# Kernel tuning notes

Hardware: AMD Instinct MI355X
Metric: run time of the kernel (lower is better)

The kernel has to match this reference:

```python
import jax, jax.numpy as jnp
import numpy as np
import math

D_MODEL = 1024
N_HEADS = 16
HEAD_DIM = D_MODEL // N_HEADS
BATCH = 2
SEQ = 2048


def setup_inputs() -> dict:
    key = jax.random.key(0)
    ks = jax.random.split(key, 6)
    x = jax.random.normal(ks[0], (BATCH, SEQ, D_MODEL), dtype=jnp.float32)
    # causal additive mask, finite large negative
    causal = jnp.tril(jnp.ones((SEQ, SEQ), dtype=bool))
    attn_mask = jnp.where(causal, 0.0, -1e9).astype(jnp.float32)[None, None, :, :]
    s = 1.0 / math.sqrt(D_MODEL)
    W_qkv = jax.random.uniform(ks[1], (3 * D_MODEL, D_MODEL), jnp.float32, -s, s)
    b_qkv = jax.random.uniform(ks[2], (3 * D_MODEL,), jnp.float32, -s, s)
    W_out = jax.random.uniform(ks[3], (D_MODEL, D_MODEL), jnp.float32, -s, s)
    b_out = jax.random.uniform(ks[4], (D_MODEL,), jnp.float32, -s, s)
    return {"x": x, "attn_mask": attn_mask, "W_qkv": W_qkv, "b_qkv": b_qkv,
            "W_out": W_out, "b_out": b_out}


def reference(x, attn_mask, W_qkv, b_qkv, W_out, b_out):
    batch, seq, _ = x.shape
    # torch Linear: x @ W^T + b
    qkv = x @ W_qkv.T + b_qkv                              # [B,S,3D]
    qkv = qkv.reshape(batch, seq, 3, N_HEADS, HEAD_DIM)
    qkv = jnp.transpose(qkv, (2, 0, 3, 1, 4))              # [3,B,H,S,hd]
    q, k, v = qkv[0], qkv[1], qkv[2]
    scores = jnp.einsum('bhsd,bhtd->bhst', q, k) / math.sqrt(HEAD_DIM)
    scores = scores + attn_mask
    attn = jax.nn.softmax(scores, axis=-1)                 # dropout p=0 (eval)
    context = jnp.einsum('bhst,bhtd->bhsd', attn, v)       # [B,H,S,hd]
    context = jnp.transpose(context, (0, 2, 1, 3)).reshape(batch, seq, D_MODEL)
    return context @ W_out.T + b_out
```

## Files before the change

### kernel.cpp

```cpp
#include <hip/hip_runtime.h>
#include <hip/hip_bf16.h>

#define BATCH 2
#define SEQ 2048
#define DMODEL 1024
#define NHEADS 16
#define HDIM 64
#define MROWS (BATCH*SEQ)

typedef short bf16x8_t __attribute__((ext_vector_type(8)));
typedef float f32x4_t __attribute__((ext_vector_type(4)));

union Frag { uint4 u; bf16x8_t b; };

__device__ __forceinline__ unsigned short f2bf(float f) {
  union { __hip_bfloat16 h; unsigned short s; } u;
  u.h = __float2bfloat16(f);
  return u.s;
}

__device__ __forceinline__ void gload16(const unsigned short* g, unsigned short* l) {
  __builtin_amdgcn_global_load_lds(
      (const __attribute__((address_space(1))) unsigned int*)(const void*)g,
      (__attribute__((address_space(3))) unsigned int*)(void*)l,
      16, 0, 0);
}

__global__ void cvt_kernel(const float* __restrict__ in,
                           unsigned short* __restrict__ out, int n4) {
  for (int i = blockIdx.x * blockDim.x + threadIdx.x; i < n4;
       i += gridDim.x * blockDim.x) {
    float4 v = reinterpret_cast<const float4*>(in)[i];
    ushort4 o;
    o.x = f2bf(v.x); o.y = f2bf(v.y); o.z = f2bf(v.z); o.w = f2bf(v.w);
    reinterpret_cast<ushort4*>(out)[i] = o;
  }
}

#define QSCALE 0.18033688011112042f


__launch_bounds__(256)
__global__ void qkv_gemm_kernel(const unsigned short* __restrict__ A,
                                const unsigned short* __restrict__ Bw,
                                const float* __restrict__ bias,
                                unsigned short* __restrict__ qb,
                                unsigned short* __restrict__ kb,
                                unsigned short* __restrict__ vb) {
  __shared__ __align__(16) unsigned short As[128 * 32];
  __shared__ __align__(16) unsigned short Bs[128 * 32];
  const int tid = threadIdx.x;
  const int w = tid >> 6, lane = tid & 63;
  const int rr = lane & 15, cg = lane >> 4;
  const int wr = w >> 1, wc = w & 1;
  const int bm = blockIdx.x * 128, bn = blockIdx.y * 128;

  const int cid0 = (w * 2) * 64 + lane, cid1 = (w * 2 + 1) * 64 + lane;
  const int rowA0 = cid0 >> 2, kc0 = cid0 & 3;
  const int rowA1 = cid1 >> 2, kc1 = cid1 & 3;
  const unsigned short* gA0 = A + (size_t)(bm + rowA0) * DMODEL + kc0 * 8;
  const unsigned short* gA1 = A + (size_t)(bm + rowA1) * DMODEL + kc1 * 8;
  const unsigned short* gB0 = Bw + (size_t)(bn + rowA0) * DMODEL + kc0 * 8;
  const unsigned short* gB1 = Bw + (size_t)(bn + rowA1) * DMODEL + kc1 * 8;
  unsigned short* lA0 = As + (w * 2) * 512;
  unsigned short* lA1 = As + (w * 2 + 1) * 512;
  unsigned short* lB0 = Bs + (w * 2) * 512;
  unsigned short* lB1 = Bs + (w * 2 + 1) * 512;

  f32x4_t acc[4][4];
#pragma unroll
  for (int i = 0; i < 4; ++i)
#pragma unroll
    for (int j = 0; j < 4; ++j) acc[i][j] = (f32x4_t){0.f, 0.f, 0.f, 0.f};

  for (int k0 = 0; k0 < DMODEL; k0 += 32) {
    __syncthreads();
    gload16(gA0 + k0, lA0);
    gload16(gA1 + k0, lA1);
    gload16(gB0 + k0, lB0);
    gload16(gB1 + k0, lB1);
    __syncthreads();
    const uint4* A4 = reinterpret_cast<const uint4*>(As);
    const uint4* B4 = reinterpret_cast<const uint4*>(Bs);
    Frag af[4], bf[4];
#pragma unroll
    for (int mt = 0; mt < 4; ++mt) af[mt].u = A4[(wr * 64 + 16 * mt + rr) * 4 + cg];
#pragma unroll
    for (int nt = 0; nt < 4; ++nt) bf[nt].u = B4[(wc * 64 + 16 * nt + rr) * 4 + cg];
#pragma unroll
    for (int mt = 0; mt < 4; ++mt)
#pragma unroll
      for (int nt = 0; nt < 4; ++nt)
        acc[mt][nt] = __builtin_amdgcn_mfma_f32_16x16x32_bf16(af[mt].b, bf[nt].b, acc[mt][nt], 0, 0, 0);
  }

#pragma unroll
  for (int nt = 0; nt < 4; ++nt) {
    const int m = bn + wc * 64 + 16 * nt + rr;
    const float bv = bias[m];
    const int which = m >> 10;
    const int h = (m & 1023) >> 6;
    const int d = m & 63;
#pragma unroll
    for (int mt = 0; mt < 4; ++mt) {
#pragma unroll
      for (int r = 0; r < 4; ++r) {
        const int n = bm + wr * 64 + 16 * mt + cg * 4 + r;
        const int b = n >> 11, sq = n & (SEQ - 1);
        const int bh = b * NHEADS + h;
        float val = acc[mt][nt][r] + bv;
        if (which == 0) {
          qb[((size_t)bh * SEQ + sq) * HDIM + d] = f2bf(val * QSCALE);
        } else if (which == 1) {
          kb[((size_t)bh * SEQ + sq) * HDIM + d] = f2bf(val);
        } else {
          vb[((size_t)bh * HDIM + d) * SEQ + sq] = f2bf(val);
        }
      }
    }
  }
}

__launch_bounds__(256)
__global__ void out_gemm_kernel(const unsigned short* __restrict__ A,
                                const unsigned short* __restrict__ Bw,
                                const float* __restrict__ bias,
                                float* __restrict__ out) {
  __shared__ __align__(16) unsigned short As[128 * 32];
  __shared__ __align__(16) unsigned short Bs[128 * 32];
  const int tid = threadIdx.x;
  const int w = tid >> 6, lane = tid & 63;
  const int rr = lane & 15, cg = lane >> 4;
  const int wr = w >> 1, wc = w & 1;
  const int bm = blockIdx.x * 128, bn = blockIdx.y * 128;

  const int cid0 = (w * 2) * 64 + lane, cid1 = (w * 2 + 1) * 64 + lane;
  const int rowA0 = cid0 >> 2, kc0 = cid0 & 3;
  const int rowA1 = cid1 >> 2, kc1 = cid1 & 3;
  const unsigned short* gA0 = A + (size_t)(bm + rowA0) * DMODEL + kc0 * 8;
  const unsigned short* gA1 = A + (size_t)(bm + rowA1) * DMODEL + kc1 * 8;
  const unsigned short* gB0 = Bw + (size_t)(bn + rowA0) * DMODEL + kc0 * 8;
  const unsigned short* gB1 = Bw + (size_t)(bn + rowA1) * DMODEL + kc1 * 8;
  unsigned short* lA0 = As + (w * 2) * 512;
  unsigned short* lA1 = As + (w * 2 + 1) * 512;
  unsigned short* lB0 = Bs + (w * 2) * 512;
  unsigned short* lB1 = Bs + (w * 2 + 1) * 512;

  f32x4_t acc[4][4];
#pragma unroll
  for (int i = 0; i < 4; ++i)
#pragma unroll
    for (int j = 0; j < 4; ++j) acc[i][j] = (f32x4_t){0.f, 0.f, 0.f, 0.f};

  for (int k0 = 0; k0 < DMODEL; k0 += 32) {
    __syncthreads();
    gload16(gA0 + k0, lA0);
    gload16(gA1 + k0, lA1);
    gload16(gB0 + k0, lB0);
    gload16(gB1 + k0, lB1);
    __syncthreads();
    const uint4* A4 = reinterpret_cast<const uint4*>(As);
    const uint4* B4 = reinterpret_cast<const uint4*>(Bs);
    Frag af[4], bf[4];
#pragma unroll
    for (int mt = 0; mt < 4; ++mt) af[mt].u = A4[(wr * 64 + 16 * mt + rr) * 4 + cg];
#pragma unroll
    for (int nt = 0; nt < 4; ++nt) bf[nt].u = B4[(wc * 64 + 16 * nt + rr) * 4 + cg];
#pragma unroll
    for (int mt = 0; mt < 4; ++mt)
#pragma unroll
      for (int nt = 0; nt < 4; ++nt)
        acc[mt][nt] = __builtin_amdgcn_mfma_f32_16x16x32_bf16(af[mt].b, bf[nt].b, acc[mt][nt], 0, 0, 0);
  }

#pragma unroll
  for (int nt = 0; nt < 4; ++nt) {
    const int m = bn + wc * 64 + 16 * nt + rr;
    const float bv = bias[m];
#pragma unroll
    for (int mt = 0; mt < 4; ++mt) {
#pragma unroll
      for (int r = 0; r < 4; ++r) {
        const int n = bm + wr * 64 + 16 * mt + cg * 4 + r;
        out[(size_t)n * DMODEL + m] = acc[mt][nt][r] + bv;
      }
    }
  }
}

__launch_bounds__(256, 4)
__global__ void attn_kernel(const unsigned short* __restrict__ qb,
                            const unsigned short* __restrict__ kb,
                            const unsigned short* __restrict__ vb,
                            unsigned short* __restrict__ ctx) {
  __shared__ __align__(16) uint4 Ks[2][512];
  __shared__ __align__(16) uint4 Vs[2][512];

  const int tid = threadIdx.x;
  const int w = tid >> 6, lane = tid & 63;
  const int rr = lane & 15, cg = lane >> 4;
  const int rxw = rr & 7;
  const int bh = blockIdx.x;
  const int c = 31 - blockIdx.y;

  const unsigned short* Kbh = kb + (size_t)bh * SEQ * HDIM;
  const unsigned short* Vbh = vb + (size_t)bh * HDIM * SEQ;

  const int j0 = w * 2, j1 = w * 2 + 1;
  const int cid0 = j0 * 64 + lane, cid1 = j1 * 64 + lane;
  const int row0 = cid0 >> 3, ch0 = cid0 & 7;
  const int row1 = cid1 >> 3, ch1 = cid1 & 7;
  const int kOff0 = row0 * HDIM + ((ch0 ^ (row0 & 7)) << 3);
  const int kOff1 = row1 * HDIM + ((ch1 ^ (row1 & 7)) << 3);
  const int vOff0 = row0 * SEQ + ((ch0 ^ (row0 & 7)) << 3);
  const int vOff1 = row1 * SEQ + ((ch1 ^ (row1 & 7)) << 3);

#define STAGE(bi, tb_) do {                                             \
    const unsigned short* Kt_ = Kbh + (size_t)(tb_) * HDIM;             \
    const unsigned short* Vt_ = Vbh + (tb_);                            \
    unsigned short* kl_ = (unsigned short*)&Ks[bi][0];                  \
    unsigned short* vl_ = (unsigned short*)&Vs[bi][0];                  \
    gload16(Kt_ + kOff0, kl_ + j0 * 512);                               \
    gload16(Kt_ + kOff1, kl_ + j1 * 512);                               \
    gload16(Vt_ + vOff0, vl_ + j0 * 512);                               \
    gload16(Vt_ + vOff1, vl_ + j1 * 512);                               \
  } while (0)

  const int b = bh >> 4, h = bh & 15;
  const int s_base = c * 64 + w * 16;
  const int nt = c + 1;

  STAGE(0, 0);

  Frag q0, q1;
  {
    const unsigned short* qrow = qb + ((size_t)bh * SEQ + (s_base + rr)) * HDIM;
    q0.u = *reinterpret_cast<const uint4*>(qrow + cg * 8);
    q1.u = *reinterpret_cast<const uint4*>(qrow + 32 + cg * 8);
  }

  f32x4_t acc[4];
#pragma unroll
  for (int i = 0; i < 4; ++i) acc[i] = (f32x4_t){0.f, 0.f, 0.f, 0.f};
  float mreg = -1e30f;
  float lp = 0.f;

  for (int t = 0; t < nt; ++t) {
    __syncthreads();
    if (t + 1 < nt) STAGE((t + 1) & 1, (t + 1) * 64);
    const uint4* Kt = &Ks[t & 1][0];
    const uint4* Vt = &Vs[t & 1][0];

    f32x4_t s[4];
    __builtin_amdgcn_s_setprio(1);
#pragma unroll
    for (int st = 0; st < 4; ++st) {
      s[st] = (f32x4_t){0.f, 0.f, 0.f, 0.f};
      Frag kf;
      kf.u = Kt[(st * 16 + rr) * 8 + (cg ^ rxw)];
      s[st] = __builtin_amdgcn_mfma_f32_16x16x32_bf16(kf.b, q0.b, s[st], 0, 0, 0);
      kf.u = Kt[(st * 16 + rr) * 8 + ((4 + cg) ^ rxw)];
      s[st] = __builtin_amdgcn_mfma_f32_16x16x32_bf16(kf.b, q1.b, s[st], 0, 0, 0);
    }
    __builtin_amdgcn_s_setprio(0);

    if (t == nt - 1) {
#pragma unroll
      for (int st = 0; st < 4; ++st)
#pragma unroll
        for (int r = 0; r < 4; ++r)
          if (st * 16 + cg * 4 + r > w * 16 + rr) s[st][r] = -1e30f;
    }

    float mx = s[0][0];
#pragma unroll
    for (int st = 0; st < 4; ++st)
#pragma unroll
      for (int r = 0; r < 4; ++r) mx = fmaxf(mx, s[st][r]);
    if (__any(mx > mreg + 11.0f)) {
      float m = fmaxf(mx, __shfl_xor(mx, 16));
      m = fmaxf(m, __shfl_xor(m, 32));
      m = fmaxf(m, mreg);
      const float alpha = exp2f(mreg - m);
      mreg = m;
      lp *= alpha;
      float av[4];
#pragma unroll
      for (int r = 0; r < 4; ++r) av[r] = __shfl(alpha, cg * 4 + r);
#pragma unroll
      for (int dt = 0; dt < 4; ++dt)
#pragma unroll
        for (int r = 0; r < 4; ++r) acc[dt][r] *= av[r];
    }

    float pv[4][4];
#pragma unroll
    for (int st = 0; st < 4; ++st)
#pragma unroll
      for (int r = 0; r < 4; ++r) {
        pv[st][r] = exp2f(s[st][r] - mreg);
        lp += pv[st][r];
      }

    unsigned int uu[4][2];
#pragma unroll
    for (int st = 0; st < 4; ++st)
#pragma unroll
      for (int i = 0; i < 2; ++i)
        asm("v_cvt_pk_bf16_f32 %0, %1, %2"
            : "=v"(uu[st][i]) : "v"(pv[st][2 * i]), "v"(pv[st][2 * i + 1]));

    Frag pA0, pA1;
#pragma unroll
    for (int s2 = 0; s2 < 2; ++s2) {
#pragma unroll
      for (int i = 0; i < 2; ++i) {
        unsigned int x = uu[2 * s2][i], y = uu[2 * s2 + 1][i];
        asm("v_permlane32_swap_b32 %0, %1" : "+v"(x), "+v"(y));
        asm("v_permlane16_swap_b32 %0, %1" : "+v"(x), "+v"(y));
        if (s2 == 0) { pA0.u[i] = x; pA0.u[2 + i] = y; }
        else         { pA1.u[i] = x; pA1.u[2 + i] = y; }
      }
    }

    __builtin_amdgcn_s_setprio(1);
#pragma unroll
    for (int dt = 0; dt < 4; ++dt) {
      Frag vf;
      vf.u = Vt[(dt * 16 + rr) * 8 + (cg ^ rxw)];
      acc[dt] = __builtin_amdgcn_mfma_f32_16x16x32_bf16(pA0.b, vf.b, acc[dt], 0, 0, 0);
      vf.u = Vt[(dt * 16 + rr) * 8 + ((4 + cg) ^ rxw)];
      acc[dt] = __builtin_amdgcn_mfma_f32_16x16x32_bf16(pA1.b, vf.b, acc[dt], 0, 0, 0);
    }
    __builtin_amdgcn_s_setprio(0);
  }

  float ls = lp + __shfl_xor(lp, 16);
  ls += __shfl_xor(ls, 32);
  const float inv = 1.0f / ls;
  float iv[4];
#pragma unroll
  for (int r = 0; r < 4; ++r) iv[r] = __shfl(inv, cg * 4 + r);
#pragma unroll
  for (int r = 0; r < 4; ++r) {
    const int sq = s_base + cg * 4 + r;
    unsigned short* crow = ctx + (size_t)(b * SEQ + sq) * DMODEL + h * HDIM;
#pragma unroll
    for (int dt = 0; dt < 4; ++dt)
      crow[dt * 16 + rr] = f2bf(acc[dt][r] * iv[r]);
  }
#undef STAGE
}

extern "C" void kernel_launch(void* const* d_in, const int* in_sizes, int n_in,
                              void* d_out, int out_size, void* d_ws, size_t ws_size,
                              hipStream_t stream) {
  const float* x    = (const float*)d_in[0];
  const float* Wqkv = (const float*)d_in[2];
  const float* bqkv = (const float*)d_in[3];
  const float* Wout = (const float*)d_in[4];
  const float* bout = (const float*)d_in[5];
  float* out = (float*)d_out;

  unsigned short* ws    = (unsigned short*)d_ws;
  unsigned short* xb    = ws;
  unsigned short* wqkvb = xb + (size_t)MROWS * DMODEL;
  unsigned short* woutb = wqkvb + (size_t)3 * DMODEL * DMODEL;
  unsigned short* qbuf  = woutb + (size_t)DMODEL * DMODEL;
  unsigned short* kbuf  = qbuf + (size_t)BATCH * NHEADS * SEQ * HDIM;
  unsigned short* vbuf  = kbuf + (size_t)BATCH * NHEADS * SEQ * HDIM;
  unsigned short* ctx   = vbuf + (size_t)BATCH * NHEADS * SEQ * HDIM;

  cvt_kernel<<<1024, 256, 0, stream>>>(x, xb, MROWS * DMODEL / 4);
  cvt_kernel<<<1024, 256, 0, stream>>>(Wqkv, wqkvb, 3 * DMODEL * DMODEL / 4);
  cvt_kernel<<<256, 256, 0, stream>>>(Wout, woutb, DMODEL * DMODEL / 4);

  qkv_gemm_kernel<<<dim3(MROWS / 128, 3 * DMODEL / 128), 256, 0, stream>>>(
      xb, wqkvb, bqkv, qbuf, kbuf, vbuf);

  attn_kernel<<<dim3(BATCH * NHEADS, SEQ / 64), 256, 0, stream>>>(
      qbuf, kbuf, vbuf, ctx);

  out_gemm_kernel<<<dim3(MROWS / 128, DMODEL / 128), 256, 0, stream>>>(
      ctx, woutb, bout, out);
}
```

Measured before the change: 114.8 us.

## Halve attention block size, load V from global, fuse conversion kernels

The attention kernel now uses 128-thread blocks covering 32 query rows, so there are twice as many blocks and causal work is balanced more finely. V tiles are no longer staged through LDS: each wave reads its V fragments straight from global memory into registers, and K staging is rebalanced across two waves. The row max uses v_max3 and the probability buffer reuses the score registers. The three fp32-to-bf16 conversion launches become one kernel with branching on index. The risks are uncoalesced, per-wave redundant global V loads and extra K reloads per query row.

```diff
diff --git a/kernel.cpp b/kernel.cpp
--- a/kernel.cpp
+++ b/kernel.cpp
@@ -19,6 +19,12 @@
   return u.s;
 }
 
+__device__ __forceinline__ float max3f(float a, float b, float c) {
+  float d;
+  asm("v_max3_f32 %0, %1, %2, %3" : "=v"(d) : "v"(a), "v"(b), "v"(c));
+  return d;
+}
+
 __device__ __forceinline__ void gload16(const unsigned short* g, unsigned short* l) {
   __builtin_amdgcn_global_load_lds(
       (const __attribute__((address_space(1))) unsigned int*)(const void*)g,
@@ -26,14 +32,22 @@
       16, 0, 0);
 }
 
-__global__ void cvt_kernel(const float* __restrict__ in,
-                           unsigned short* __restrict__ out, int n4) {
-  for (int i = blockIdx.x * blockDim.x + threadIdx.x; i < n4;
+__global__ void cvt3_kernel(const float* __restrict__ a, const float* __restrict__ b,
+                            const float* __restrict__ c,
+                            unsigned short* __restrict__ oa, unsigned short* __restrict__ ob,
+                            unsigned short* __restrict__ oc,
+                            int na, int nb, int nc) {
+  const int n = na + nb + nc;
+  for (int i = blockIdx.x * blockDim.x + threadIdx.x; i < n;
        i += gridDim.x * blockDim.x) {
-    float4 v = reinterpret_cast<const float4*>(in)[i];
+    const float* src; unsigned short* dst; int j;
+    if (i < na)           { src = a; dst = oa; j = i; }
+    else if (i < na + nb) { src = b; dst = ob; j = i - na; }
+    else                  { src = c; dst = oc; j = i - na - nb; }
+    float4 v = reinterpret_cast<const float4*>(src)[j];
     ushort4 o;
     o.x = f2bf(v.x); o.y = f2bf(v.y); o.z = f2bf(v.z); o.w = f2bf(v.w);
-    reinterpret_cast<ushort4*>(out)[i] = o;
+    reinterpret_cast<ushort4*>(dst)[j] = o;
   }
 }
 
@@ -188,47 +202,44 @@
   }
 }
 
-__launch_bounds__(256, 4)
+__launch_bounds__(128, 4)
 __global__ void attn_kernel(const unsigned short* __restrict__ qb,
                             const unsigned short* __restrict__ kb,
                             const unsigned short* __restrict__ vb,
                             unsigned short* __restrict__ ctx) {
   __shared__ __align__(16) uint4 Ks[2][512];
-  __shared__ __align__(16) uint4 Vs[2][512];
 
   const int tid = threadIdx.x;
   const int w = tid >> 6, lane = tid & 63;
   const int rr = lane & 15, cg = lane >> 4;
   const int rxw = rr & 7;
   const int bh = blockIdx.x;
-  const int c = 31 - blockIdx.y;
+  const int h = 63 - blockIdx.y;
+  const int b = bh >> 4, hd = bh & 15;
 
   const unsigned short* Kbh = kb + (size_t)bh * SEQ * HDIM;
   const unsigned short* Vbh = vb + (size_t)bh * HDIM * SEQ;
 
-  const int j0 = w * 2, j1 = w * 2 + 1;
-  const int cid0 = j0 * 64 + lane, cid1 = j1 * 64 + lane;
-  const int row0 = cid0 >> 3, ch0 = cid0 & 7;
-  const int row1 = cid1 >> 3, ch1 = cid1 & 7;
-  const int kOff0 = row0 * HDIM + ((ch0 ^ (row0 & 7)) << 3);
-  const int kOff1 = row1 * HDIM + ((ch1 ^ (row1 & 7)) << 3);
-  const int vOff0 = row0 * SEQ + ((ch0 ^ (row0 & 7)) << 3);
-  const int vOff1 = row1 * SEQ + ((ch1 ^ (row1 & 7)) << 3);
+  int kOff[4];
+#pragma unroll
+  for (int j = 0; j < 4; ++j) {
+    const int cid = (2 * j + w) * 64 + lane;
+    const int row = cid >> 3, ch = cid & 7;
+    kOff[j] = row * HDIM + ((ch ^ (row & 7)) << 3);
+  }
 
 #define STAGE(bi, tb_) do {                                             \
     const unsigned short* Kt_ = Kbh + (size_t)(tb_) * HDIM;             \
-    const unsigned short* Vt_ = Vbh + (tb_);                            \
-    unsigned short* kl_ = (unsigned short*)&Ks[bi][0];                  \
-    unsigned short* vl_ = (unsigned short*)&Vs[bi][0];                  \
-    gload16(Kt_ + kOff0, kl_ + j0 * 512);                               \
-    gload16(Kt_ + kOff1, kl_ + j1 * 512);                               \
-    gload16(Vt_ + vOff0, vl_ + j0 * 512);                               \
-    gload16(Vt_ + vOff1, vl_ + j1 * 512);                               \
+    unsigned short* kl_ = (unsigned short*)&Ks[bi][0] + w * 512;        \
+    gload16(Kt_ + kOff[0], kl_);                                        \
+    gload16(Kt_ + kOff[1], kl_ + 1024);                                 \
+    gload16(Kt_ + kOff[2], kl_ + 2048);                                 \
+    gload16(Kt_ + kOff[3], kl_ + 3072);                                 \
   } while (0)
 
-  const int b = bh >> 4, h = bh & 15;
-  const int s_base = c * 64 + w * 16;
-  const int nt = c + 1;
+  const int s_base = h * 32 + w * 16;
+  const int T = (h >> 1) + 1;
+  const int lim = 32 * (h & 1) + w * 16 + rr;
 
   STAGE(0, 0);
 
@@ -245,11 +256,18 @@
   float mreg = -1e30f;
   float lp = 0.f;
 
-  for (int t = 0; t < nt; ++t) {
+  for (int t = 0; t < T; ++t) {
     __syncthreads();
-    if (t + 1 < nt) STAGE((t + 1) & 1, (t + 1) * 64);
+    if (t + 1 < T) STAGE((t + 1) & 1, (t + 1) * 64);
     const uint4* Kt = &Ks[t & 1][0];
-    const uint4* Vt = &Vs[t & 1][0];
+    const unsigned short* Vt = Vbh + t * 64;
+
+    Frag vr[4][2];
+#pragma unroll
+    for (int dt = 0; dt < 4; ++dt) {
+      vr[dt][0].u = *reinterpret_cast<const uint4*>(Vt + (size_t)(dt * 16 + rr) * SEQ + cg * 8);
+      vr[dt][1].u = *reinterpret_cast<const uint4*>(Vt + (size_t)(dt * 16 + rr) * SEQ + 32 + cg * 8);
+    }
 
     f32x4_t s[4];
     __builtin_amdgcn_s_setprio(1);
@@ -264,19 +282,22 @@
     }
     __builtin_amdgcn_s_setprio(0);
 
-    if (t == nt - 1) {
+    if (t == T - 1) {
 #pragma unroll
       for (int st = 0; st < 4; ++st)
 #pragma unroll
         for (int r = 0; r < 4; ++r)
-          if (st * 16 + cg * 4 + r > w * 16 + rr) s[st][r] = -1e30f;
-    }
-
-    float mx = s[0][0];
-#pragma unroll
-    for (int st = 0; st < 4; ++st)
-#pragma unroll
-      for (int r = 0; r < 4; ++r) mx = fmaxf(mx, s[st][r]);
+          if (st * 16 + cg * 4 + r > lim) s[st][r] = -1e30f;
+    }
+
+    float mx = max3f(s[0][0], s[0][1], s[0][2]);
+    mx = max3f(mx, s[0][3], s[1][0]);
+    mx = max3f(mx, s[1][1], s[1][2]);
+    mx = max3f(mx, s[1][3], s[2][0]);
+    mx = max3f(mx, s[2][1], s[2][2]);
+    mx = max3f(mx, s[2][3], s[3][0]);
+    mx = max3f(mx, s[3][1], s[3][2]);
+    mx = fmaxf(mx, s[3][3]);
     if (__any(mx > mreg + 11.0f)) {
       float m = fmaxf(mx, __shfl_xor(mx, 16));
       m = fmaxf(m, __shfl_xor(m, 32));
@@ -293,13 +314,12 @@
         for (int r = 0; r < 4; ++r) acc[dt][r] *= av[r];
     }
 
-    float pv[4][4];
 #pragma unroll
     for (int st = 0; st < 4; ++st)
 #pragma unroll
       for (int r = 0; r < 4; ++r) {
-        pv[st][r] = exp2f(s[st][r] - mreg);
-        lp += pv[st][r];
+        s[st][r] = exp2f(s[st][r] - mreg);
+        lp += s[st][r];
       }
 
     unsigned int uu[4][2];
@@ -308,7 +328,7 @@
 #pragma unroll
       for (int i = 0; i < 2; ++i)
         asm("v_cvt_pk_bf16_f32 %0, %1, %2"
-            : "=v"(uu[st][i]) : "v"(pv[st][2 * i]), "v"(pv[st][2 * i + 1]));
+            : "=v"(uu[st][i]) : "v"(s[st][2 * i]), "v"(s[st][2 * i + 1]));
 
     Frag pA0, pA1;
 #pragma unroll
@@ -326,11 +346,8 @@
     __builtin_amdgcn_s_setprio(1);
 #pragma unroll
     for (int dt = 0; dt < 4; ++dt) {
-      Frag vf;
-      vf.u = Vt[(dt * 16 + rr) * 8 + (cg ^ rxw)];
-      acc[dt] = __builtin_amdgcn_mfma_f32_16x16x32_bf16(pA0.b, vf.b, acc[dt], 0, 0, 0);
-      vf.u = Vt[(dt * 16 + rr) * 8 + ((4 + cg) ^ rxw)];
-      acc[dt] = __builtin_amdgcn_mfma_f32_16x16x32_bf16(pA1.b, vf.b, acc[dt], 0, 0, 0);
+      acc[dt] = __builtin_amdgcn_mfma_f32_16x16x32_bf16(pA0.b, vr[dt][0].b, acc[dt], 0, 0, 0);
+      acc[dt] = __builtin_amdgcn_mfma_f32_16x16x32_bf16(pA1.b, vr[dt][1].b, acc[dt], 0, 0, 0);
     }
     __builtin_amdgcn_s_setprio(0);
   }
@@ -344,7 +361,7 @@
 #pragma unroll
   for (int r = 0; r < 4; ++r) {
     const int sq = s_base + cg * 4 + r;
-    unsigned short* crow = ctx + (size_t)(b * SEQ + sq) * DMODEL + h * HDIM;
+    unsigned short* crow = ctx + (size_t)(b * SEQ + sq) * DMODEL + hd * HDIM;
 #pragma unroll
     for (int dt = 0; dt < 4; ++dt)
       crow[dt * 16 + rr] = f2bf(acc[dt][r] * iv[r]);
@@ -371,14 +388,14 @@
   unsigned short* vbuf  = kbuf + (size_t)BATCH * NHEADS * SEQ * HDIM;
   unsigned short* ctx   = vbuf + (size_t)BATCH * NHEADS * SEQ * HDIM;
 
-  cvt_kernel<<<1024, 256, 0, stream>>>(x, xb, MROWS * DMODEL / 4);
-  cvt_kernel<<<1024, 256, 0, stream>>>(Wqkv, wqkvb, 3 * DMODEL * DMODEL / 4);
-  cvt_kernel<<<256, 256, 0, stream>>>(Wout, woutb, DMODEL * DMODEL / 4);
+  cvt3_kernel<<<2048, 256, 0, stream>>>(
+      x, Wqkv, Wout, xb, wqkvb, woutb,
+      MROWS * DMODEL / 4, 3 * DMODEL * DMODEL / 4, DMODEL * DMODEL / 4);
 
   qkv_gemm_kernel<<<dim3(MROWS / 128, 3 * DMODEL / 128), 256, 0, stream>>>(
       xb, wqkvb, bqkv, qbuf, kbuf, vbuf);
 
-  attn_kernel<<<dim3(BATCH * NHEADS, SEQ / 64), 256, 0, stream>>>(
+  attn_kernel<<<dim3(BATCH * NHEADS, 64), 128, 0, stream>>>(
       qbuf, kbuf, vbuf, ctx);
 
   out_gemm_kernel<<<dim3(MROWS / 128, DMODEL / 128), 256, 0, stream>>>(
```

After: 148.2 us. +29.1%, slower.
